# Kernel optimization log

Measured on AMD Instinct MI355X. Metric: run time of the kernel, lower is better.

## Reference

```python
import jax, jax.numpy as jnp
import numpy as np

EMBED_DIM = 128
NUM_HEADS = 4
HEAD_DIM = EMBED_DIM // NUM_HEADS


def setup_inputs() -> dict:
    key = jax.random.key(0)
    ks = jax.random.split(key, 12)
    B, N, D = 4, 4096, EMBED_DIM
    s = 1.0 / np.sqrt(D)
    inp = {
        "query": jax.random.normal(ks[0], (B, N, D), dtype=jnp.float32),
        "key": jax.random.normal(ks[1], (B, N, D), dtype=jnp.float32),
        "value": jax.random.normal(ks[2], (B, N, D), dtype=jnp.float32),
        "Wq": jax.random.uniform(ks[3], (D, D), jnp.float32, -s, s),
        "bq": jax.random.uniform(ks[4], (D,), jnp.float32, -s, s),
        "Wk": jax.random.uniform(ks[5], (D, D), jnp.float32, -s, s),
        "bk": jax.random.uniform(ks[6], (D,), jnp.float32, -s, s),
        "Wv": jax.random.uniform(ks[7], (D, D), jnp.float32, -s, s),
        "bv": jax.random.uniform(ks[8], (D,), jnp.float32, -s, s),
        "Wo": jax.random.uniform(ks[9], (D, D), jnp.float32, -s, s),
        "bo": jax.random.uniform(ks[10], (D,), jnp.float32, -s, s),
    }
    return inp


def reference(query, key, value, Wq, bq, Wk, bk, Wv, bv, Wo, bo):
    B, N, D = query.shape
    H, Dh = NUM_HEADS, HEAD_DIM
    scale = Dh ** -0.5
    # Linear projections (torch Linear: x @ W.T + b), split heads -> [B, H, N, Dh]
    Q = (query @ Wq.T + bq).reshape(B, N, H, Dh).transpose(0, 2, 1, 3)
    K = (key @ Wk.T + bk).reshape(B, N, H, Dh).transpose(0, 2, 1, 3)
    V = (value @ Wv.T + bv).reshape(B, N, H, Dh).transpose(0, 2, 1, 3)
    # Attention scores [B, H, N, N]
    scores = jnp.einsum('bhqd,bhkd->bhqk', Q, K) * scale
    attn = jax.nn.softmax(scores, axis=-1)
    ctx = jnp.einsum('bhqk,bhkd->bhqd', attn, V)  # [B, H, N, Dh]
    ctx = ctx.transpose(0, 2, 1, 3).reshape(B, N, D)
    return ctx @ Wo.T + bo
```

## Files before the change

### kernel.cpp

```cpp
#include <hip/hip_runtime.h>
#include <hip/hip_bf16.h>

#define N_SEQ 4096
#define DIM   128
#define NH    4
#define DH    32
#define BATCH 4

#define QSCALE 0.25503495870989204f

typedef __bf16 bf16x8 __attribute__((ext_vector_type(8)));
typedef __bf16 bf16x2 __attribute__((ext_vector_type(2)));
typedef __bf16 bf16x4 __attribute__((ext_vector_type(4)));
typedef float  f32x4  __attribute__((ext_vector_type(4)));

#define MFMA(a, b, c) __builtin_amdgcn_mfma_f32_16x16x32_bf16((a), (b), (c), 0, 0, 0)

static __device__ __forceinline__ bf16x8 cvt8(const float* __restrict__ p) {
    const float4* f4 = reinterpret_cast<const float4*>(p);
    float4 a = f4[0], b = f4[1];
    bf16x8 r;
    r[0] = (__bf16)a.x; r[1] = (__bf16)a.y; r[2] = (__bf16)a.z; r[3] = (__bf16)a.w;
    r[4] = (__bf16)b.x; r[5] = (__bf16)b.y; r[6] = (__bf16)b.z; r[7] = (__bf16)b.w;
    return r;
}

static __device__ __forceinline__ f32x4 exp4(f32x4 s) {
    f32x4 r;
    r[0] = __builtin_amdgcn_exp2f(s[0]);
    r[1] = __builtin_amdgcn_exp2f(s[1]);
    r[2] = __builtin_amdgcn_exp2f(s[2]);
    r[3] = __builtin_amdgcn_exp2f(s[3]);
    return r;
}

static __device__ __forceinline__ bf16x8 pack8(f32x4 a, f32x4 b) {
    bf16x8 o;
    o[0] = (__bf16)a[0]; o[1] = (__bf16)a[1];
    o[2] = (__bf16)a[2]; o[3] = (__bf16)a[3];
    o[4] = (__bf16)b[0]; o[5] = (__bf16)b[1];
    o[6] = (__bf16)b[2]; o[7] = (__bf16)b[3];
    return o;
}

__global__ __launch_bounds__(256) void proj_qkv(
    const float* __restrict__ xq, const float* __restrict__ xk, const float* __restrict__ xv,
    const float* __restrict__ Wq, const float* __restrict__ Wk, const float* __restrict__ Wv,
    const float* __restrict__ bq, const float* __restrict__ bk, const float* __restrict__ bv,
    __bf16* __restrict__ Qs, __bf16* __restrict__ Kb, __bf16* __restrict__ Vt)
{
    __shared__ __align__(16) char wlds[34816];
    const int z = blockIdx.z;
    const float* x    = (z == 0) ? xq : ((z == 1) ? xk : xv);
    const float* Wf   = (z == 0) ? Wq : ((z == 1) ? Wk : Wv);
    const float* bias = (z == 0) ? bq : ((z == 1) ? bk : bv);
    const int b    = blockIdx.y;
    const int tid  = threadIdx.x;
    const int wave = tid >> 6, lane = tid & 63;
    const int quad = lane >> 4, l15 = lane & 15;
    const int n0   = blockIdx.x * 64 + wave * 16;

    {
        const int r = tid >> 1, half = tid & 1;
        const float* wsrc = Wf + r * DIM + half * 64;
        char* wdst = wlds + r * 272 + half * 128;
        #pragma unroll
        for (int i = 0; i < 8; i++)
            *(bf16x8*)(wdst + i * 16) = cvt8(wsrc + i * 8);
    }

    bf16x8 a[4];
    const float* xrow = x + (b * N_SEQ + n0 + l15) * DIM + quad * 8;
    a[0] = cvt8(xrow);      a[1] = cvt8(xrow + 32);
    a[2] = cvt8(xrow + 64); a[3] = cvt8(xrow + 96);
    __syncthreads();

    const int n = n0 + l15;
    for (int t = 0; t < 8; t++) {
        const char* wr = wlds + (t * 16 + l15) * 272 + quad * 16;
        bf16x8 w0 = *(const bf16x8*)(wr);
        bf16x8 w1 = *(const bf16x8*)(wr + 64);
        bf16x8 w2 = *(const bf16x8*)(wr + 128);
        bf16x8 w3 = *(const bf16x8*)(wr + 192);

        f32x4 acc = {0.f, 0.f, 0.f, 0.f};
        acc = MFMA(w0, a[0], acc);
        acc = MFMA(w1, a[1], acc);
        acc = MFMA(w2, a[2], acc);
        acc = MFMA(w3, a[3], acc);

        const int d0 = t * 16 + quad * 4;
        if (z == 0) {
            const int h = d0 >> 5, dh0 = d0 & 31;
            bf16x4 q4;
            #pragma unroll
            for (int r = 0; r < 4; r++)
                q4[r] = (__bf16)((acc[r] + bias[d0 + r]) * QSCALE);
            *(bf16x4*)(Qs + ((b * NH + h) * N_SEQ + n) * DH + dh0) = q4;
        } else if (z == 1) {
            const int h = d0 >> 5, dh0 = d0 & 31;
            bf16x4 k4;
            #pragma unroll
            for (int r = 0; r < 4; r++)
                k4[r] = (__bf16)(acc[r] + bias[d0 + r]);
            *(bf16x4*)(Kb + ((b * NH + h) * N_SEQ + n) * DH + dh0) = k4;
        } else {
            const int nl = n & 63;
            const int np = (n & ~63) | (nl & 35) | ((nl & 12) << 1) | ((nl & 16) >> 2);
            #pragma unroll
            for (int r = 0; r < 4; r++) {
                const int d = d0 + r, h = d >> 5, dh = d & 31;
                Vt[((b * NH + h) * DH + dh) * N_SEQ + np] = (__bf16)(acc[r] + bias[d]);
            }
        }
    }
}

__global__ __launch_bounds__(512, 4) void flash_attn(
    const __bf16* __restrict__ Qs, const __bf16* __restrict__ Kb,
    const __bf16* __restrict__ Vt, __bf16* __restrict__ ctxb)
{
    __shared__ __align__(16) char smem[77824];
    char* const Kbase = smem;
    char* const Vbase = smem + 40960;

    const int bid  = blockIdx.x;
    const int bh   = bid & 15;
    const int qc   = bid >> 4;
    const int tid  = threadIdx.x;
    const int wave = tid >> 6, lane = tid & 63;
    const int quad = lane >> 4, l15 = lane & 15;
    const int qh   = wave & 3, kh = wave >> 2;
    const int n0   = qc * 128 + qh * 32;
    const int KH   = 2048;

    const __bf16* Qp = Qs + (bh * N_SEQ + n0) * DH;
    bf16x8 qf[2];
    qf[0] = *(const bf16x8*)(Qp + l15 * DH + quad * 8);
    qf[1] = *(const bf16x8*)(Qp + (16 + l15) * DH + quad * 8);

    const int s = tid & 255;
    const bool isK = (tid < 256);
    const __bf16* gsrc;
    char* ldsb;
    int kofs, gstr, bstr, tstr;
    size_t gmul;
    if (isK) {
        gsrc = Kb + (size_t)bh * N_SEQ * DH + (s >> 2) * DH + (s & 3) * 8;
        ldsb = Kbase; kofs = (s >> 2) * 80 + (s & 3) * 16;
        gstr = 20480; bstr = 10240; tstr = 5120; gmul = DH;
    } else {
        gsrc = Vt + ((size_t)bh * DH + (s >> 3)) * N_SEQ + (s & 7) * 8;
        ldsb = Vbase; kofs = (s >> 3) * 144 + (s & 7) * 16;
        gstr = 18432; bstr = 9216; tstr = 4608; gmul = 1;
    }

    {
        #pragma unroll
        for (int g = 0; g < 2; g++) {
            #pragma unroll
            for (int t = 0; t < 2; t++) {
                bf16x8 r = *(const bf16x8*)(gsrc + (size_t)(g * KH + t * 64) * gmul);
                *(bf16x8*)(ldsb + g * gstr + t * tstr + kofs) = r;
            }
        }
    }
    __syncthreads();

    char* const Kme = Kbase + kh * 20480;
    char* const Vme = Vbase + kh * 18432;

    f32x4 c[2][2];
    const f32x4 z4 = {0.f, 0.f, 0.f, 0.f};
    c[0][0] = z4; c[0][1] = z4; c[1][0] = z4; c[1][1] = z4;
    float l[2] = {0.f, 0.f};

    for (int kbb = 0; kbb < KH / 128; kbb++) {
        const int cur = kbb & 1;
        const char* Kc = Kme + cur * 10240;
        const char* Vc = Vme + cur * 9216;

        const int kn = (kbb + 1) & (KH / 128 - 1);
        bf16x8 pre[2][2];
        #pragma unroll
        for (int g = 0; g < 2; g++) {
            #pragma unroll
            for (int t = 0; t < 2; t++)
                pre[g][t] = *(const bf16x8*)(gsrc + (size_t)(g * KH + kn * 128 + t * 64) * gmul);
        }

        #pragma unroll
        for (int t = 0; t < 2; t++) {
            const char* Kt  = Kc + t * 5120;
            const char* Vtl = Vc + t * 4608;

            bf16x8 kf0 = *(const bf16x8*)(Kt + l15 * 80 + quad * 16);
            bf16x8 kf1 = *(const bf16x8*)(Kt + (16 + l15) * 80 + quad * 16);
            bf16x8 kf2 = *(const bf16x8*)(Kt + (32 + l15) * 80 + quad * 16);
            bf16x8 kf3 = *(const bf16x8*)(Kt + (48 + l15) * 80 + quad * 16);

            bf16x8 pf[2][2];
            #pragma unroll
            for (int q = 0; q < 2; q++) {
                f32x4 sa = MFMA(kf0, qf[q], z4);
                f32x4 sb = MFMA(kf1, qf[q], z4);
                f32x4 sc = MFMA(kf2, qf[q], z4);
                f32x4 sd = MFMA(kf3, qf[q], z4);
                f32x4 ea = exp4(sa), eb = exp4(sb), ec = exp4(sc), ed = exp4(sd);
                l[q] += ((ea[0]+ea[1])+(ea[2]+ea[3])) + ((eb[0]+eb[1])+(eb[2]+eb[3]))
                      + ((ec[0]+ec[1])+(ec[2]+ec[3])) + ((ed[0]+ed[1])+(ed[2]+ed[3]));
                pf[q][0] = pack8(ea, eb);
                pf[q][1] = pack8(ec, ed);
            }

            bf16x8 vf00 = *(const bf16x8*)(Vtl + l15 * 144 + quad * 16);
            bf16x8 vf10 = *(const bf16x8*)(Vtl + (16 + l15) * 144 + quad * 16);
            bf16x8 vf01 = *(const bf16x8*)(Vtl + l15 * 144 + 64 + quad * 16);
            bf16x8 vf11 = *(const bf16x8*)(Vtl + (16 + l15) * 144 + 64 + quad * 16);

            #pragma unroll
            for (int q = 0; q < 2; q++) {
                c[q][0] = MFMA(vf00, pf[q][0], c[q][0]);
                c[q][1] = MFMA(vf10, pf[q][0], c[q][1]);
                c[q][0] = MFMA(vf01, pf[q][1], c[q][0]);
                c[q][1] = MFMA(vf11, pf[q][1], c[q][1]);
            }
        }

        #pragma unroll
        for (int g = 0; g < 2; g++) {
            #pragma unroll
            for (int t = 0; t < 2; t++)
                *(bf16x8*)(ldsb + g * gstr + (cur ^ 1) * bstr + t * tstr + kofs) = pre[g][t];
        }
        __syncthreads();
    }

    #pragma unroll
    for (int q = 0; q < 2; q++) {
        l[q] += __shfl_xor(l[q], 16);
        l[q] += __shfl_xor(l[q], 32);
    }

    if (kh == 1) {
        char* dst = smem + (qh * 64 + lane) * 80;
        #pragma unroll
        for (int q = 0; q < 2; q++) {
            *(f32x4*)(dst + q * 32)      = c[q][0];
            *(f32x4*)(dst + q * 32 + 16) = c[q][1];
        }
        float2 lv = {l[0], l[1]};
        *(float2*)(dst + 64) = lv;
    }
    __syncthreads();
    if (kh == 0) {
        const char* src = smem + (qh * 64 + lane) * 80;
        float2 lp = *(const float2*)(src + 64);
        const float lpa[2] = {lp.x, lp.y};
        const int b = bh >> 2, h = bh & 3;
        #pragma unroll
        for (int q = 0; q < 2; q++) {
            c[q][0] += *(const f32x4*)(src + q * 32);
            c[q][1] += *(const f32x4*)(src + q * 32 + 16);
            const float inv = 1.0f / (l[q] + lpa[q]);
            const int qg = n0 + q * 16 + l15;
            __bf16* dst = ctxb + ((size_t)(b * N_SEQ + qg)) * DIM + h * DH + quad * 4;
            #pragma unroll
            for (int dt = 0; dt < 2; dt++) {
                f32x4 cc = c[q][dt];
                bf16x2 e0 = {(__bf16)(cc[0] * inv), (__bf16)(cc[1] * inv)};
                bf16x2 e1 = {(__bf16)(cc[2] * inv), (__bf16)(cc[3] * inv)};
                *(bf16x2*)(dst + dt * 16)     = e0;
                *(bf16x2*)(dst + dt * 16 + 2) = e1;
            }
        }
    }
}

__global__ __launch_bounds__(256) void out_proj(
    const __bf16* __restrict__ ctxb, const float* __restrict__ Wo,
    const float* __restrict__ bo, float* __restrict__ out)
{
    __shared__ __align__(16) char wlds[34816];
    const int b    = blockIdx.y;
    const int tid  = threadIdx.x;
    const int wave = tid >> 6, lane = tid & 63;
    const int quad = lane >> 4, l15 = lane & 15;
    const int n0   = blockIdx.x * 64 + wave * 16;

    {
        const int r = tid >> 1, half = tid & 1;
        const float* wsrc = Wo + r * DIM + half * 64;
        char* wdst = wlds + r * 272 + half * 128;
        #pragma unroll
        for (int i = 0; i < 8; i++)
            *(bf16x8*)(wdst + i * 16) = cvt8(wsrc + i * 8);
    }

    bf16x8 a[4];
    const __bf16* crow = ctxb + (b * N_SEQ + n0 + l15) * DIM + quad * 8;
    a[0] = *(const bf16x8*)(crow);
    a[1] = *(const bf16x8*)(crow + 32);
    a[2] = *(const bf16x8*)(crow + 64);
    a[3] = *(const bf16x8*)(crow + 96);
    __syncthreads();

    const int n = n0 + l15;
    for (int t = 0; t < 8; t++) {
        const char* wr = wlds + (t * 16 + l15) * 272 + quad * 16;
        bf16x8 w0 = *(const bf16x8*)(wr);
        bf16x8 w1 = *(const bf16x8*)(wr + 64);
        bf16x8 w2 = *(const bf16x8*)(wr + 128);
        bf16x8 w3 = *(const bf16x8*)(wr + 192);

        f32x4 acc = {0.f, 0.f, 0.f, 0.f};
        acc = MFMA(w0, a[0], acc);
        acc = MFMA(w1, a[1], acc);
        acc = MFMA(w2, a[2], acc);
        acc = MFMA(w3, a[3], acc);

        const int d0 = t * 16 + quad * 4;
        float4 o;
        o.x = acc[0] + bo[d0];
        o.y = acc[1] + bo[d0 + 1];
        o.z = acc[2] + bo[d0 + 2];
        o.w = acc[3] + bo[d0 + 3];
        *(float4*)(out + (b * N_SEQ + n) * DIM + d0) = o;
    }
}

extern "C" void kernel_launch(void* const* d_in, const int* in_sizes, int n_in,
                              void* d_out, int out_size, void* d_ws, size_t ws_size,
                              hipStream_t stream)
{
    const float* query = (const float*)d_in[0];
    const float* key   = (const float*)d_in[1];
    const float* value = (const float*)d_in[2];
    const float* Wq = (const float*)d_in[3];
    const float* bq = (const float*)d_in[4];
    const float* Wk = (const float*)d_in[5];
    const float* bk = (const float*)d_in[6];
    const float* Wv = (const float*)d_in[7];
    const float* bv = (const float*)d_in[8];
    const float* Wo = (const float*)d_in[9];
    const float* bo = (const float*)d_in[10];
    float* out = (float*)d_out;

    char* ws = (char*)d_ws;
    const size_t e = (size_t)BATCH * N_SEQ * DIM;
    __bf16* Qs   = (__bf16*)(ws);
    __bf16* Kb   = (__bf16*)(ws + 2 * e);
    __bf16* Vt   = (__bf16*)(ws + 4 * e);
    __bf16* ctxb = (__bf16*)(ws + 6 * e);

    proj_qkv<<<dim3(64, BATCH, 3), 256, 0, stream>>>(
        query, key, value, Wq, Wk, Wv, bq, bk, bv, Qs, Kb, Vt);
    flash_attn<<<dim3(512), 512, 0, stream>>>(Qs, Kb, Vt, ctxb);
    out_proj<<<dim3(64, BATCH), 256, 0, stream>>>(ctxb, Wo, bo, out);
}
```

Measured before the change: 158.2 us.

## Shrink attention blocks to 256 threads and compute row sums via MFMA

Each attention block now covers 64 queries with 4 waves instead of 128 with 8, and the grid doubles to 1024 blocks, so LDS per block halves and more blocks can be resident. The softmax denominator is no longer summed with scalar adds and lane shuffles; an extra MFMA against an all-ones operand accumulates it alongside the context. s_setprio hints are wrapped around the MFMA sections to favour matrix issue across waves. The trade-off is two extra MFMAs per q tile per step, K/V loaded from global twice as often overall because of the smaller query tiles, and a barrier every 64 keys instead of every 128.

```diff
diff --git a/kernel.cpp b/kernel.cpp
--- a/kernel.cpp
+++ b/kernel.cpp
@@ -116,13 +116,13 @@
     }
 }
 
-__global__ __launch_bounds__(512, 4) void flash_attn(
+__global__ __launch_bounds__(256, 4) void flash_attn(
     const __bf16* __restrict__ Qs, const __bf16* __restrict__ Kb,
     const __bf16* __restrict__ Vt, __bf16* __restrict__ ctxb)
 {
-    __shared__ __align__(16) char smem[77824];
+    __shared__ __align__(16) char smem[38912];
     char* const Kbase = smem;
-    char* const Vbase = smem + 40960;
+    char* const Vbase = smem + 20480;
 
     const int bid  = blockIdx.x;
     const int bh   = bid & 15;
@@ -130,8 +130,8 @@
     const int tid  = threadIdx.x;
     const int wave = tid >> 6, lane = tid & 63;
     const int quad = lane >> 4, l15 = lane & 15;
-    const int qh   = wave & 3, kh = wave >> 2;
-    const int n0   = qc * 128 + qh * 32;
+    const int qh   = wave & 1, kh = wave >> 1;
+    const int n0   = qc * 64 + qh * 32;
     const int KH   = 2048;
 
     const __bf16* Qp = Qs + (bh * N_SEQ + n0) * DH;
@@ -139,107 +139,88 @@
     qf[0] = *(const bf16x8*)(Qp + l15 * DH + quad * 8);
     qf[1] = *(const bf16x8*)(Qp + (16 + l15) * DH + quad * 8);
 
-    const int s = tid & 255;
-    const bool isK = (tid < 256);
-    const __bf16* gsrc;
-    char* ldsb;
-    int kofs, gstr, bstr, tstr;
-    size_t gmul;
-    if (isK) {
-        gsrc = Kb + (size_t)bh * N_SEQ * DH + (s >> 2) * DH + (s & 3) * 8;
-        ldsb = Kbase; kofs = (s >> 2) * 80 + (s & 3) * 16;
-        gstr = 20480; bstr = 10240; tstr = 5120; gmul = DH;
-    } else {
-        gsrc = Vt + ((size_t)bh * DH + (s >> 3)) * N_SEQ + (s & 7) * 8;
-        ldsb = Vbase; kofs = (s >> 3) * 144 + (s & 7) * 16;
-        gstr = 18432; bstr = 9216; tstr = 4608; gmul = 1;
-    }
+    bf16x8 ones;
+    #pragma unroll
+    for (int i = 0; i < 8; i++) ones[i] = (__bf16)1.0f;
+
+    const int r_ = tid >> 2, c_ = tid & 3;
+    const __bf16* gK = Kb + (size_t)bh * N_SEQ * DH + r_ * DH + c_ * 8;
+    const __bf16* gV = Vt + ((size_t)bh * DH + (tid >> 3)) * N_SEQ + (tid & 7) * 8;
+    const int kofsK = r_ * 80 + c_ * 16;
+    const int kofsV = (tid >> 3) * 144 + (tid & 7) * 16;
 
     {
         #pragma unroll
         for (int g = 0; g < 2; g++) {
-            #pragma unroll
-            for (int t = 0; t < 2; t++) {
-                bf16x8 r = *(const bf16x8*)(gsrc + (size_t)(g * KH + t * 64) * gmul);
-                *(bf16x8*)(ldsb + g * gstr + t * tstr + kofs) = r;
-            }
+            bf16x8 kr = *(const bf16x8*)(gK + (size_t)(g * KH) * DH);
+            bf16x8 vr = *(const bf16x8*)(gV + g * KH);
+            *(bf16x8*)(Kbase + g * 10240 + kofsK) = kr;
+            *(bf16x8*)(Vbase + g * 9216  + kofsV) = vr;
         }
     }
     __syncthreads();
 
-    char* const Kme = Kbase + kh * 20480;
-    char* const Vme = Vbase + kh * 18432;
+    char* const Kme = Kbase + kh * 10240;
+    char* const Vme = Vbase + kh * 9216;
 
     f32x4 c[2][2];
-    const f32x4 z4 = {0.f, 0.f, 0.f, 0.f};
+    f32x4 cl[2];
+    const f32x4 z4 = {0.f,0.f,0.f,0.f};
     c[0][0] = z4; c[0][1] = z4; c[1][0] = z4; c[1][1] = z4;
-    float l[2] = {0.f, 0.f};
-
-    for (int kbb = 0; kbb < KH / 128; kbb++) {
-        const int cur = kbb & 1;
-        const char* Kc = Kme + cur * 10240;
-        const char* Vc = Vme + cur * 9216;
-
-        const int kn = (kbb + 1) & (KH / 128 - 1);
-        bf16x8 pre[2][2];
-        #pragma unroll
-        for (int g = 0; g < 2; g++) {
-            #pragma unroll
-            for (int t = 0; t < 2; t++)
-                pre[g][t] = *(const bf16x8*)(gsrc + (size_t)(g * KH + kn * 128 + t * 64) * gmul);
-        }
-
-        #pragma unroll
-        for (int t = 0; t < 2; t++) {
-            const char* Kt  = Kc + t * 5120;
-            const char* Vtl = Vc + t * 4608;
-
-            bf16x8 kf0 = *(const bf16x8*)(Kt + l15 * 80 + quad * 16);
-            bf16x8 kf1 = *(const bf16x8*)(Kt + (16 + l15) * 80 + quad * 16);
-            bf16x8 kf2 = *(const bf16x8*)(Kt + (32 + l15) * 80 + quad * 16);
-            bf16x8 kf3 = *(const bf16x8*)(Kt + (48 + l15) * 80 + quad * 16);
-
-            bf16x8 pf[2][2];
-            #pragma unroll
-            for (int q = 0; q < 2; q++) {
-                f32x4 sa = MFMA(kf0, qf[q], z4);
-                f32x4 sb = MFMA(kf1, qf[q], z4);
-                f32x4 sc = MFMA(kf2, qf[q], z4);
-                f32x4 sd = MFMA(kf3, qf[q], z4);
-                f32x4 ea = exp4(sa), eb = exp4(sb), ec = exp4(sc), ed = exp4(sd);
-                l[q] += ((ea[0]+ea[1])+(ea[2]+ea[3])) + ((eb[0]+eb[1])+(eb[2]+eb[3]))
-                      + ((ec[0]+ec[1])+(ec[2]+ec[3])) + ((ed[0]+ed[1])+(ed[2]+ed[3]));
-                pf[q][0] = pack8(ea, eb);
-                pf[q][1] = pack8(ec, ed);
-            }
-
-            bf16x8 vf00 = *(const bf16x8*)(Vtl + l15 * 144 + quad * 16);
-            bf16x8 vf10 = *(const bf16x8*)(Vtl + (16 + l15) * 144 + quad * 16);
-            bf16x8 vf01 = *(const bf16x8*)(Vtl + l15 * 144 + 64 + quad * 16);
-            bf16x8 vf11 = *(const bf16x8*)(Vtl + (16 + l15) * 144 + 64 + quad * 16);
-
-            #pragma unroll
-            for (int q = 0; q < 2; q++) {
-                c[q][0] = MFMA(vf00, pf[q][0], c[q][0]);
-                c[q][1] = MFMA(vf10, pf[q][0], c[q][1]);
-                c[q][0] = MFMA(vf01, pf[q][1], c[q][0]);
-                c[q][1] = MFMA(vf11, pf[q][1], c[q][1]);
-            }
-        }
-
-        #pragma unroll
-        for (int g = 0; g < 2; g++) {
-            #pragma unroll
-            for (int t = 0; t < 2; t++)
-                *(bf16x8*)(ldsb + g * gstr + (cur ^ 1) * bstr + t * tstr + kofs) = pre[g][t];
-        }
+    cl[0] = z4; cl[1] = z4;
+
+    for (int t = 0; t < 32; t++) {
+        const int cur = t & 1;
+        const char* Kt  = Kme + cur * 5120;
+        const char* Vtl = Vme + cur * 4608;
+
+        const int kn = (t + 1) & 31;
+        bf16x8 kr0 = *(const bf16x8*)(gK + (size_t)(kn * 64) * DH);
+        bf16x8 kr1 = *(const bf16x8*)(gK + (size_t)(KH + kn * 64) * DH);
+        bf16x8 vr0 = *(const bf16x8*)(gV + kn * 64);
+        bf16x8 vr1 = *(const bf16x8*)(gV + KH + kn * 64);
+
+        bf16x8 kf0 = *(const bf16x8*)(Kt + l15 * 80 + quad * 16);
+        bf16x8 kf1 = *(const bf16x8*)(Kt + (16 + l15) * 80 + quad * 16);
+        bf16x8 kf2 = *(const bf16x8*)(Kt + (32 + l15) * 80 + quad * 16);
+        bf16x8 kf3 = *(const bf16x8*)(Kt + (48 + l15) * 80 + quad * 16);
+
+        bf16x8 pf[2][2];
+        #pragma unroll
+        for (int q = 0; q < 2; q++) {
+            __builtin_amdgcn_s_setprio(1);
+            f32x4 sa = MFMA(kf0, qf[q], z4);
+            f32x4 sb = MFMA(kf1, qf[q], z4);
+            f32x4 sc = MFMA(kf2, qf[q], z4);
+            f32x4 sd = MFMA(kf3, qf[q], z4);
+            __builtin_amdgcn_s_setprio(0);
+            f32x4 ea = exp4(sa), eb = exp4(sb), ec = exp4(sc), ed = exp4(sd);
+            pf[q][0] = pack8(ea, eb);
+            pf[q][1] = pack8(ec, ed);
+        }
+
+        bf16x8 vf0 = *(const bf16x8*)(Vtl + l15 * 144 + quad * 16);
+        bf16x8 vf1 = *(const bf16x8*)(Vtl + (16 + l15) * 144 + quad * 16);
+        bf16x8 vf2 = *(const bf16x8*)(Vtl + l15 * 144 + 64 + quad * 16);
+        bf16x8 vf3 = *(const bf16x8*)(Vtl + (16 + l15) * 144 + 64 + quad * 16);
+
+        __builtin_amdgcn_s_setprio(1);
+        #pragma unroll
+        for (int q = 0; q < 2; q++) {
+            c[q][0] = MFMA(vf0, pf[q][0], c[q][0]);
+            c[q][1] = MFMA(vf1, pf[q][0], c[q][1]);
+            c[q][0] = MFMA(vf2, pf[q][1], c[q][0]);
+            c[q][1] = MFMA(vf3, pf[q][1], c[q][1]);
+            cl[q]   = MFMA(ones, pf[q][0], cl[q]);
+            cl[q]   = MFMA(ones, pf[q][1], cl[q]);
+        }
+        __builtin_amdgcn_s_setprio(0);
+
+        *(bf16x8*)(Kbase + (cur ^ 1) * 5120 + kofsK)          = kr0;
+        *(bf16x8*)(Kbase + 10240 + (cur ^ 1) * 5120 + kofsK)  = kr1;
+        *(bf16x8*)(Vbase + (cur ^ 1) * 4608 + kofsV)          = vr0;
+        *(bf16x8*)(Vbase + 9216 + (cur ^ 1) * 4608 + kofsV)   = vr1;
         __syncthreads();
-    }
-
-    #pragma unroll
-    for (int q = 0; q < 2; q++) {
-        l[q] += __shfl_xor(l[q], 16);
-        l[q] += __shfl_xor(l[q], 32);
     }
 
     if (kh == 1) {
@@ -249,7 +230,7 @@
             *(f32x4*)(dst + q * 32)      = c[q][0];
             *(f32x4*)(dst + q * 32 + 16) = c[q][1];
         }
-        float2 lv = {l[0], l[1]};
+        float2 lv = {cl[0][0], cl[1][0]};
         *(float2*)(dst + 64) = lv;
     }
     __syncthreads();
@@ -262,7 +243,7 @@
         for (int q = 0; q < 2; q++) {
             c[q][0] += *(const f32x4*)(src + q * 32);
             c[q][1] += *(const f32x4*)(src + q * 32 + 16);
-            const float inv = 1.0f / (l[q] + lpa[q]);
+            const float inv = 1.0f / (cl[q][0] + lpa[q]);
             const int qg = n0 + q * 16 + l15;
             __bf16* dst = ctxb + ((size_t)(b * N_SEQ + qg)) * DIM + h * DH + quad * 4;
             #pragma unroll
@@ -355,6 +336,6 @@
 
     proj_qkv<<<dim3(64, BATCH, 3), 256, 0, stream>>>(
         query, key, value, Wq, Wk, Wv, bq, bk, bv, Qs, Kb, Vt);
-    flash_attn<<<dim3(512), 512, 0, stream>>>(Qs, Kb, Vt, ctxb);
+    flash_attn<<<dim3(1024), 256, 0, stream>>>(Qs, Kb, Vt, ctxb);
     out_proj<<<dim3(64, BATCH), 256, 0, stream>>>(ctxb, Wo, bo, out);
 }
```

Result: faster. 149.7 us (-5.4%).
